# Optimization experiments

Hardware: AMD Instinct MI355X
Metric: run time of the kernel (lower is better)

Reference implementation:

```python
import jax, jax.numpy as jnp
import numpy as np

GAMMA = 0.7


def setup_inputs() -> dict:
    key = jax.random.key(0)
    k1, k2, k3 = jax.random.split(key, 3)
    K, N, M = 8, 2_000_000, 50_000
    states_x = jax.random.normal(k1, (K, N, 3), dtype=jnp.float32)
    x_target = jax.random.normal(k2, (N, 3), dtype=jnp.float32)
    molecule_id = jnp.sort(jax.random.randint(k3, (N,), 0, M, dtype=jnp.int64))
    return {
        "states_x": states_x,
        "x_target": x_target,
        "molecule_id": molecule_id,
        "num_molecules": M,
    }


def reference(states_x, x_target, molecule_id, num_molecules):
    # states_x: (K, N, 3) = refinement states 1..K (state 0 is already dropped)
    # x_target: (N, 3); molecule_id: (N,) segment ids
    K = states_x.shape[0]
    dtype = x_target.dtype
    # exponential weights gamma^(K-1-k), normalized
    w = jnp.power(jnp.asarray(GAMMA, dtype), (K - 1) - jnp.arange(K, dtype=dtype))
    w = w / w.sum()
    # per-atom squared distance per state: (K, N)
    sq = ((states_x - x_target[None]) ** 2).sum(axis=-1)
    # segment-reduce over molecules: sums (M, K), counts (M,)
    sums = jax.ops.segment_sum(sq.T, molecule_id, num_segments=num_molecules)
    counts = jax.ops.segment_sum(
        jnp.ones((molecule_id.shape[0],), dtype=dtype), molecule_id,
        num_segments=num_molecules)
    valid = counts > 0  # pt.unique only iterates over ids that appear
    means = sums / jnp.maximum(counts, 1)[:, None]  # (M, K) per-molecule mean sq dist
    per_state = (means * valid[:, None].astype(dtype)).sum(axis=0) / valid.sum().astype(dtype)
    return (w * per_state).sum()
```

## Files before the change

### kernel.cpp

```cpp
#include <hip/hip_runtime.h>

#define GAMMA 0.7f
static constexpr int K = 8;
static constexpr int B = 512;
static constexpr int P = B * 4;
static constexpr int NW = B / 64;


__global__ void __launch_bounds__(B)
main_fused(const float* __restrict__ sx,
           const float* __restrict__ xt,
           const int* __restrict__ mol,
           float* __restrict__ partials,
           int* __restrict__ bcounts,
           int N) {
    const int tid = threadIdx.x;
    const int b0  = blockIdx.x * P;
    const int n0  = b0 + tid * 4;

    __shared__ int ids[P + 2];
    __shared__ int edgeLR[2];
    int* w = ids + 1;

    int myid[4];
    if (n0 + 3 < N) {
        int4 v = *reinterpret_cast<const int4*>(mol + n0);
        myid[0] = v.x; myid[1] = v.y; myid[2] = v.z; myid[3] = v.w;
    } else {
#pragma unroll
        for (int j = 0; j < 4; ++j) {
            int n = n0 + j;
            myid[j] = (n < N) ? mol[n] : 0x7fffffff;
        }
    }
#pragma unroll
    for (int j = 0; j < 4; ++j) w[tid * 4 + j] = myid[j];
    if (tid == 0) {
        ids[0]    = (b0 == 0) ? -1 : mol[b0 - 1];
        edgeLR[0] = b0;
        edgeLR[1] = b0 + P;
    }
    if (tid == B - 1) ids[P + 1] = (b0 + P >= N) ? 0x7fffffff : mol[b0 + P];
    __syncthreads();

    const int wave = tid >> 6, lane = tid & 63;

    if (wave == 0) {
        if (b0 > 0 && ids[0] == w[0]) {
            const int id = w[0];
            int c = 0;
            for (;;) {
                int idx = b0 - 1 - (c * 64 + lane);
                bool ended = (idx < 0) || (mol[idx] != id);
                unsigned long long m = __ballot(ended);
                if (m) {
                    if (lane == 0) {
                        int l0 = __ffsll((long long)m) - 1;
                        edgeLR[0] = b0 - 1 - (c * 64 + l0) + 1;
                    }
                    break;
                }
                ++c;
            }
        }
    } else if (wave == NW - 1) {
        if (b0 + P < N && ids[P + 1] == w[P - 1]) {
            const int id = w[P - 1];
            int c = 0;
            for (;;) {
                int idx = b0 + P + (c * 64 + lane);
                bool ended = (idx >= N) || (mol[idx] != id);
                unsigned long long m = __ballot(ended);
                if (m) {
                    if (lane == 0) {
                        int l0 = __ffsll((long long)m) - 1;
                        edgeLR[1] = b0 + P + (c * 64 + l0);
                    }
                    break;
                }
                ++c;
            }
        }
    }

    int sj[4], ej[4];
    int nb = 0;
#pragma unroll
    for (int j = 0; j < 4; ++j) {
        const int p  = tid * 4 + j;
        const int id = myid[j];
        const bool valid = (b0 + p < N);
        const int prevv = (j > 0) ? myid[j - 1] : ids[p];
        if (valid && prevv != id) ++nb;
        if (j > 0 && myid[j - 1] == id) { sj[j] = sj[j - 1]; ej[j] = ej[j - 1]; continue; }
        if (!valid) { sj[j] = 0; ej[j] = 1; continue; }

        int slo = 0, shi = p, elo = p + 1, ehi = P;
        while (slo < shi || elo < ehi) {
            if (slo < shi) {
                int m = (slo + shi) >> 1;
                if (w[m] < id) slo = m + 1; else shi = m;
            }
            if (elo < ehi) {
                int m = (elo + ehi) >> 1;
                if (w[m] <= id) elo = m + 1; else ehi = m;
            }
        }
        sj[j] = slo; ej[j] = elo;
    }
    __syncthreads();

    const int eL = edgeLR[0], eR = edgeLR[1];
    float inv[4];
#pragma unroll
    for (int j = 0; j < 4; ++j) {
        const bool valid = (b0 + tid * 4 + j < N);
        const int gstart = (sj[j] == 0) ? eL : b0 + sj[j];
        const int gend   = (ej[j] == P) ? eR : b0 + ej[j];
        inv[j] = valid ? 1.0f / (float)(gend - gstart) : 0.0f;
    }

    float acc[K];
#pragma unroll
    for (int k = 0; k < K; ++k) acc[k] = 0.0f;

    if (n0 + 3 < N) {
        const float4* tp = reinterpret_cast<const float4*>(xt + (size_t)n0 * 3);
        float4 t0 = tp[0], t1 = tp[1], t2 = tp[2];
        float tg[12] = {t0.x, t0.y, t0.z, t0.w, t1.x, t1.y,
                        t1.z, t1.w, t2.x, t2.y, t2.z, t2.w};
#pragma unroll
        for (int k = 0; k < K; ++k) {
            const float4* sp = reinterpret_cast<const float4*>(
                sx + (size_t)k * N * 3 + (size_t)n0 * 3);
            float4 s0 = sp[0], s1 = sp[1], s2 = sp[2];
            float sv[12] = {s0.x, s0.y, s0.z, s0.w, s1.x, s1.y,
                            s1.z, s1.w, s2.x, s2.y, s2.z, s2.w};
#pragma unroll
            for (int j = 0; j < 4; ++j) {
                float dx = sv[3 * j + 0] - tg[3 * j + 0];
                float dy = sv[3 * j + 1] - tg[3 * j + 1];
                float dz = sv[3 * j + 2] - tg[3 * j + 2];
                acc[k] += (dx * dx + dy * dy + dz * dz) * inv[j];
            }
        }
    } else if (n0 < N) {
        for (int n = n0; n < N; ++n) {
            const int j = n - n0;
            float tx = xt[(size_t)n * 3 + 0];
            float ty = xt[(size_t)n * 3 + 1];
            float tz = xt[(size_t)n * 3 + 2];
#pragma unroll
            for (int k = 0; k < K; ++k) {
                const float* s = sx + (size_t)k * N * 3 + (size_t)n * 3;
                float dx = s[0] - tx, dy = s[1] - ty, dz = s[2] - tz;
                acc[k] += (dx * dx + dy * dy + dz * dz) * inv[j];
            }
        }
    }

#pragma unroll
    for (int k = 0; k < K; ++k)
#pragma unroll
        for (int off = 32; off > 0; off >>= 1)
            acc[k] += __shfl_down(acc[k], off, 64);
#pragma unroll
    for (int off = 32; off > 0; off >>= 1) nb += __shfl_down(nb, off, 64);

    __shared__ float lds[NW][K];
    __shared__ int   bl[NW];
    if (lane == 0) {
        bl[wave] = nb;
#pragma unroll
        for (int k = 0; k < K; ++k) lds[wave][k] = acc[k];
    }
    __syncthreads();
    if (tid < K) {
        int k = tid;
        float s = 0.0f;
#pragma unroll
        for (int v = 0; v < NW; ++v) s += lds[v][k];
        partials[(size_t)blockIdx.x * K + k] = s;
    }
    if (tid == 0) {
        int s = 0;
#pragma unroll
        for (int v = 0; v < NW; ++v) s += bl[v];
        bcounts[blockIdx.x] = s;
    }
}

__global__ void __launch_bounds__(B)
final_kernel(const float* __restrict__ partials,
             const int* __restrict__ bcounts, int nblocks,
             float* __restrict__ out) {
    const int t = threadIdx.x;

    int vc = 0;
    for (int i = t; i < nblocks; i += B) vc += bcounts[i];
#pragma unroll
    for (int off = 32; off > 0; off >>= 1) vc += __shfl_down(vc, off, 64);

    float acc[K];
#pragma unroll
    for (int k = 0; k < K; ++k) acc[k] = 0.0f;
    for (int i = t; i < nblocks; i += B) {
        const float4* row = reinterpret_cast<const float4*>(partials + (size_t)i * K);
        float4 a = row[0], b = row[1];
        acc[0] += a.x; acc[1] += a.y; acc[2] += a.z; acc[3] += a.w;
        acc[4] += b.x; acc[5] += b.y; acc[6] += b.z; acc[7] += b.w;
    }
#pragma unroll
    for (int k = 0; k < K; ++k)
#pragma unroll
        for (int off = 32; off > 0; off >>= 1)
            acc[k] += __shfl_down(acc[k], off, 64);

    __shared__ int vlds[NW];
    __shared__ float plds[NW][K];
    const int wave = t >> 6, lane = t & 63;
    if (lane == 0) {
        vlds[wave] = vc;
#pragma unroll
        for (int k = 0; k < K; ++k) plds[wave][k] = acc[k];
    }
    __syncthreads();

    if (t == 0) {
        int V = 0;
        float ps[K];
#pragma unroll
        for (int k = 0; k < K; ++k) ps[k] = 0.0f;
#pragma unroll
        for (int v = 0; v < NW; ++v) {
            V += vlds[v];
#pragma unroll
            for (int k = 0; k < K; ++k) ps[k] += plds[v][k];
        }
        float w[K], wsum = 0.0f, g = 1.0f;
        for (int j = 0; j < K; ++j) {
            w[K - 1 - j] = g;
            wsum += g;
            g *= GAMMA;
        }
        float invV = (V > 0) ? 1.0f / (float)V : 0.0f;
        float res = 0.0f;
#pragma unroll
        for (int k = 0; k < K; ++k)
            res += (w[k] / wsum) * (ps[k] * invV);
        out[0] = res;
    }
}

extern "C" void kernel_launch(void* const* d_in, const int* in_sizes, int n_in,
                              void* d_out, int out_size, void* d_ws, size_t ws_size,
                              hipStream_t stream) {
    const float* states_x = (const float*)d_in[0];
    const float* x_target = (const float*)d_in[1];
    const int*   mol      = (const int*)d_in[2];

    const int N = in_sizes[2];
    const int nblocks = (N + P - 1) / P;

    char* ws = (char*)d_ws;
    size_t boff = (((size_t)nblocks * K * 4) + 255) & ~(size_t)255;

    float* partials = (float*)ws;
    int*   bcounts  = (int*)(ws + boff);

    main_fused<<<nblocks, B, 0, stream>>>(states_x, x_target, mol,
                                          partials, bcounts, N);
    final_kernel<<<1, B, 0, stream>>>(partials, bcounts, nblocks,
                                      (float*)d_out);
}
```

Measured before the change: 50.74 us.

## Replace final reduction kernel with fixed-point atomics and last-block finish

```diff
diff --git a/kernel.cpp b/kernel.cpp
--- a/kernel.cpp
+++ b/kernel.cpp
@@ -6,14 +6,19 @@
 static constexpr int P = B * 4;
 static constexpr int NW = B / 64;
 
+static constexpr float SCALE     = 16777216.0f;
+static constexpr float INV_SCALE = 1.0f / 16777216.0f;
+
 
 __global__ void __launch_bounds__(B)
 main_fused(const float* __restrict__ sx,
            const float* __restrict__ xt,
            const int* __restrict__ mol,
-           float* __restrict__ partials,
-           int* __restrict__ bcounts,
-           int N) {
+           unsigned long long* __restrict__ cells,
+           int* __restrict__ vcount,
+           unsigned* __restrict__ ctr,
+           float* __restrict__ out,
+           int N, int nblocks) {
     const int tid = threadIdx.x;
     const int b0  = blockIdx.x * P;
     const int n0  = b0 + tid * 4;
@@ -175,80 +180,48 @@
         for (int k = 0; k < K; ++k) lds[wave][k] = acc[k];
     }
     __syncthreads();
+
     if (tid < K) {
-        int k = tid;
         float s = 0.0f;
 #pragma unroll
-        for (int v = 0; v < NW; ++v) s += lds[v][k];
-        partials[(size_t)blockIdx.x * K + k] = s;
+        for (int v = 0; v < NW; ++v) s += lds[v][tid];
+        unsigned long long q = (unsigned long long)llrintf(s * SCALE);
+        unsigned long long old = atomicAdd(&cells[tid], q);
+        asm volatile("" :: "v"(old));
     }
     if (tid == 0) {
-        int s = 0;
-#pragma unroll
-        for (int v = 0; v < NW; ++v) s += bl[v];
-        bcounts[blockIdx.x] = s;
-    }
-}
-
-__global__ void __launch_bounds__(B)
-final_kernel(const float* __restrict__ partials,
-             const int* __restrict__ bcounts, int nblocks,
-             float* __restrict__ out) {
-    const int t = threadIdx.x;
-
-    int vc = 0;
-    for (int i = t; i < nblocks; i += B) vc += bcounts[i];
-#pragma unroll
-    for (int off = 32; off > 0; off >>= 1) vc += __shfl_down(vc, off, 64);
-
-    float acc[K];
-#pragma unroll
-    for (int k = 0; k < K; ++k) acc[k] = 0.0f;
-    for (int i = t; i < nblocks; i += B) {
-        const float4* row = reinterpret_cast<const float4*>(partials + (size_t)i * K);
-        float4 a = row[0], b = row[1];
-        acc[0] += a.x; acc[1] += a.y; acc[2] += a.z; acc[3] += a.w;
-        acc[4] += b.x; acc[5] += b.y; acc[6] += b.z; acc[7] += b.w;
-    }
-#pragma unroll
-    for (int k = 0; k < K; ++k)
-#pragma unroll
-        for (int off = 32; off > 0; off >>= 1)
-            acc[k] += __shfl_down(acc[k], off, 64);
-
-    __shared__ int vlds[NW];
-    __shared__ float plds[NW][K];
-    const int wave = t >> 6, lane = t & 63;
-    if (lane == 0) {
-        vlds[wave] = vc;
-#pragma unroll
-        for (int k = 0; k < K; ++k) plds[wave][k] = acc[k];
-    }
-    __syncthreads();
-
-    if (t == 0) {
-        int V = 0;
-        float ps[K];
-#pragma unroll
-        for (int k = 0; k < K; ++k) ps[k] = 0.0f;
-#pragma unroll
-        for (int v = 0; v < NW; ++v) {
-            V += vlds[v];
-#pragma unroll
-            for (int k = 0; k < K; ++k) ps[k] += plds[v][k];
-        }
-        float w[K], wsum = 0.0f, g = 1.0f;
-        for (int j = 0; j < K; ++j) {
-            w[K - 1 - j] = g;
-            wsum += g;
-            g *= GAMMA;
-        }
-        float invV = (V > 0) ? 1.0f / (float)V : 0.0f;
-        float res = 0.0f;
-#pragma unroll
-        for (int k = 0; k < K; ++k)
-            res += (w[k] / wsum) * (ps[k] * invV);
-        out[0] = res;
+        int sb = 0;
+#pragma unroll
+        for (int v = 0; v < NW; ++v) sb += bl[v];
+        int oldv = atomicAdd(vcount, sb);
+        asm volatile("" :: "v"(oldv));
+    }
+    asm volatile("s_waitcnt vmcnt(0)" ::: "memory");
+
+    if (tid == 0) {
+        unsigned t = atomicAdd(ctr, 1u);
+        if (t == (unsigned)nblocks - 1u) {
+            long long c[K];
+#pragma unroll
+            for (int k = 0; k < K; ++k)
+                c[k] = (long long)atomicAdd(&cells[k], 0ULL);
+            int V = atomicAdd(vcount, 0);
+
+            float wgt[K], wsum = 0.0f, g = 1.0f;
+            for (int j = 0; j < K; ++j) {
+                wgt[K - 1 - j] = g;
+                wsum += g;
+                g *= GAMMA;
+            }
+            float invV = (V > 0) ? 1.0f / (float)V : 0.0f;
+            float res = 0.0f;
+#pragma unroll
+            for (int k = 0; k < K; ++k) {
+                float ps = (float)c[k] * INV_SCALE * invV;
+                res += (wgt[k] / wsum) * ps;
+            }
+            out[0] = res;
+        }
     }
 }
 
@@ -263,13 +236,13 @@
     const int nblocks = (N + P - 1) / P;
 
     char* ws = (char*)d_ws;
-    size_t boff = (((size_t)nblocks * K * 4) + 255) & ~(size_t)255;
-
-    float* partials = (float*)ws;
-    int*   bcounts  = (int*)(ws + boff);
+    unsigned long long* cells = (unsigned long long*)ws;
+    int*      vcount = (int*)(ws + 64);
+    unsigned* ctr    = (unsigned*)(ws + 68);
+
+    hipMemsetAsync(d_ws, 0, 128, stream);
 
     main_fused<<<nblocks, B, 0, stream>>>(states_x, x_target, mol,
-                                          partials, bcounts, N);
-    final_kernel<<<1, B, 0, stream>>>(partials, bcounts, nblocks,
-                                      (float*)d_out);
+                                          cells, vcount, ctr,
+                                          (float*)d_out, N, nblocks);
 }
```

Measured after the change: 59.46 us. +17.2%, slower.
